# Optimization experiments

Hardware: AMD Instinct MI355X
Metric: run time of the kernel (lower is better)

The kernel has to match this reference:

```python
import jax, jax.numpy as jnp
import numpy as np

N, H, E, C, V, K = 4096, 256, 128, 32, 64, 20


def setup_inputs() -> dict:
    key = jax.random.key(0)
    ks = jax.random.split(key, 16)
    f = lambda k, s: jax.random.normal(k, s, dtype=jnp.float32)
    return {
        "vec": f(ks[0], (N, H)),
        "inp": f(ks[1], (N, E)),
        "h_prev": f(ks[2], (N, H)),
        "c_prev": f(ks[3], (N, H)),
        "Wlin": f(ks[4], (C, V, H)) * 0.05,
        "blin": f(ks[5], (C, V)) * 0.05,
        "Wec": f(ks[6], (2, H)) * 0.05,
        "bec": f(ks[7], (2,)) * 0.05,
        "Wrel": f(ks[8], (5, H)) * 0.05,
        "brel": f(ks[9], (5,)) * 0.05,
        "W_ih": f(ks[10], (K, 4 * H, E)) * 0.05,
        "b_ih": f(ks[11], (K, 4 * H)) * 0.05,
        "W_hh": f(ks[12], (K, 4 * H, H)) * 0.05,
        "b_hh": f(ks[13], (K, 4 * H)) * 0.05,
        "category": jax.random.randint(ks[14], (N,), 0, C, dtype=jnp.int32),
        "cell_id": jax.random.randint(ks[15], (N,), 0, K, dtype=jnp.int32),
        "true_idx": jax.random.randint(jax.random.fold_in(key, 100), (N,), 0, V, dtype=jnp.int32),
        "ec_idx": jax.random.randint(jax.random.fold_in(key, 101), (N,), 0, 2, dtype=jnp.int32),
        "rel_idx": jax.random.randint(jax.random.fold_in(key, 102), (N,), 0, 5, dtype=jnp.int32),
    }


def _ce(logits, targets):
    # per-row cross entropy (same math as nn.CrossEntropyLoss per example)
    logp = jax.nn.log_softmax(logits, axis=-1)
    return -jnp.take_along_axis(logp, targets[:, None], axis=-1)[:, 0]


def reference(vec, inp, h_prev, c_prev, Wlin, blin, Wec, bec, Wrel, brel,
              W_ih, b_ih, W_hh, b_hh, category, cell_id, true_idx, ec_idx, rel_idx):
    # --- get_log_odds: per-category tiny linear head, selected by category ---
    logits_all = jnp.einsum('nh,cvh->ncv', vec, Wlin) + blin          # [N,C,V]
    logits = jnp.take_along_axis(logits_all, category[:, None, None].astype(jnp.int32), axis=1)[:, 0]  # [N,V]
    logits_ec = vec @ Wec.T + bec                                      # [N,2]
    logits_rel = vec @ Wrel.T + brel                                   # [N,5]

    # --- calculate_loss: CE over valid children + ec + rel ---
    losses = _ce(logits, true_idx) + _ce(logits_ec, ec_idx) + _ce(logits_rel, rel_idx)  # [N]

    # --- get_next: per-child-index LSTMCell, selected by cell_id ---
    gates_all = (jnp.einsum('ne,kge->nkg', inp, W_ih)
                 + jnp.einsum('nh,kgh->nkg', h_prev, W_hh)
                 + b_ih + b_hh)                                        # [N,K,4H]
    gates = jnp.take_along_axis(gates_all, cell_id[:, None, None].astype(jnp.int32), axis=1)[:, 0]  # [N,4H]
    i, f, g, o = jnp.split(gates, 4, axis=-1)                          # torch LSTMCell gate order i,f,g,o
    c_next = jax.nn.sigmoid(f) * c_prev + jax.nn.sigmoid(i) * jnp.tanh(g)
    h_next = jax.nn.sigmoid(o) * jnp.tanh(c_next)

    # pack: [N, 1 + 2H] = loss | h_next | c_next
    return jnp.concatenate([losses[:, None], h_next, c_next], axis=-1)
```

## Files before the change

kernel.cpp:

```cpp
#include <hip/hip_runtime.h>
#include <hip/hip_bf16.h>
#include <math.h>

#define Nn 4096
#define Hdim 256
#define Edim 128
#define Cdim 32
#define Vdim 64
#define Kdim 20
#define G4H 1024
#define OUTS 513

#define SK 512
#define SC 256
#define RK_OFF 64
#define RC_OFF (RK_OFF + Kdim * SK)
#define NLI 18496
#define NSI 18497
#define ITL 18498
#define ITS (ITL + 640)

#define LSTM_REGION 592
#define LOSS_REGION 320
#define GRID (LSTM_REGION + LOSS_REGION)
#define XCHUNK 114

typedef short bf16x8 __attribute__((ext_vector_type(8)));
typedef float f32x4 __attribute__((ext_vector_type(4)));

__device__ __forceinline__ float sigmoidf_(float x) { return 1.0f / (1.0f + expf(-x)); }

__device__ __forceinline__ bf16x8 cvt8(float4 f0, float4 f1) {
    bf16x8 r;
    __hip_bfloat16 h;
    h = __float2bfloat16(f0.x); r[0] = *(short*)&h;
    h = __float2bfloat16(f0.y); r[1] = *(short*)&h;
    h = __float2bfloat16(f0.z); r[2] = *(short*)&h;
    h = __float2bfloat16(f0.w); r[3] = *(short*)&h;
    h = __float2bfloat16(f1.x); r[4] = *(short*)&h;
    h = __float2bfloat16(f1.y); r[5] = *(short*)&h;
    h = __float2bfloat16(f1.z); r[6] = *(short*)&h;
    h = __float2bfloat16(f1.w); r[7] = *(short*)&h;
    return r;
}

__device__ __forceinline__ void gl_lds16(const void* g, void* l) {
    __builtin_amdgcn_global_load_lds((const __attribute__((address_space(1))) void*)g,
                                     (__attribute__((address_space(3))) void*)l, 16, 0, 0);
}

__device__ __forceinline__ int swz(int r) { return ((r & 3) << 1) | ((r >> 2) & 1); }

__global__ __launch_bounds__(1024) void k_bucket(const int* __restrict__ cell_id,
                                                 const int* __restrict__ category,
                                                 int* __restrict__ ws) {
    __shared__ int cnt[32];
    __shared__ int off[33];
    int t = threadIdx.x;
    if (t < 32) cnt[t] = 0;
    __syncthreads();
    int i0 = t * 4;
    if (blockIdx.x == 0) {
        int4 v = ((const int4*)cell_id)[t];
        int r;
        r = atomicAdd(&cnt[v.x], 1); if (r < SK) ws[RK_OFF + v.x * SK + r] = i0 + 0;
        r = atomicAdd(&cnt[v.y], 1); if (r < SK) ws[RK_OFF + v.y * SK + r] = i0 + 1;
        r = atomicAdd(&cnt[v.z], 1); if (r < SK) ws[RK_OFF + v.z * SK + r] = i0 + 2;
        r = atomicAdd(&cnt[v.w], 1); if (r < SK) ws[RK_OFF + v.w * SK + r] = i0 + 3;
        __syncthreads();
        if (t == 0) {
            int a = 0;
            for (int kk = 0; kk < Kdim; kk++) { off[kk] = a; a += (min(cnt[kk], SK) + 31) >> 5; }
            ws[NLI] = a * 4;
        }
        __syncthreads();
        if (t < Kdim) {
            int ns = (min(cnt[t], SK) + 31) >> 5;
            int base = off[t] * 4;
            for (int hq = 0; hq < 4; hq++)
                for (int s = 0; s < ns; s++)
                    ws[ITL + base + hq * ns + s] = t | (s << 8) | (hq << 16);
        }
        if (t < 32) ws[t] = min(cnt[t], SK);
    } else {
        int4 v = ((const int4*)category)[t];
        int r;
        r = atomicAdd(&cnt[v.x], 1); if (r < SC) ws[RC_OFF + v.x * SC + r] = i0 + 0;
        r = atomicAdd(&cnt[v.y], 1); if (r < SC) ws[RC_OFF + v.y * SC + r] = i0 + 1;
        r = atomicAdd(&cnt[v.z], 1); if (r < SC) ws[RC_OFF + v.z * SC + r] = i0 + 2;
        r = atomicAdd(&cnt[v.w], 1); if (r < SC) ws[RC_OFF + v.w * SC + r] = i0 + 3;
        __syncthreads();
        if (t == 0) {
            int a = 0;
            for (int cc = 0; cc < Cdim; cc++) { off[cc] = a; a += (min(cnt[cc], SC) + 15) >> 4; }
            ws[NSI] = a;
        }
        __syncthreads();
        if (t < Cdim) {
            int ns = (min(cnt[t], SC) + 15) >> 4;
            int base = off[t];
            for (int s = 0; s < ns; s++)
                ws[ITS + base + s] = t | (s << 8);
        }
        if (t < 32) ws[32 + t] = min(cnt[t], SC);
    }
}

__global__ __launch_bounds__(256, 4) void k_main(
    const float* __restrict__ vec, const float* __restrict__ inp,
    const float* __restrict__ h_prev, const float* __restrict__ c_prev,
    const float* __restrict__ Wlin, const float* __restrict__ blin,
    const float* __restrict__ Wec, const float* __restrict__ bec,
    const float* __restrict__ Wrel, const float* __restrict__ brel,
    const float* __restrict__ W_ih, const float* __restrict__ b_ih,
    const float* __restrict__ W_hh, const float* __restrict__ b_hh,
    const int* __restrict__ true_idx, const int* __restrict__ ec_idx, const int* __restrict__ rel_idx,
    const int* __restrict__ ws,
    float* __restrict__ out)
{
    __shared__ __align__(16) char smem[36864];

    int t = threadIdx.x;
    int w = t >> 6, l = t & 63;
    int l15 = l & 15, quad = l >> 4;
    int lrow8 = l >> 3, lslot = l & 7;
    int p0 = (quad * 2) ^ swz(l15);

    int work = (blockIdx.x & 7) * XCHUNK + (blockIdx.x >> 3);

    if (work < LSTM_REGION) {
        if (work >= ws[NLI]) return;
        int item = ws[ITL + work];
        int k = item & 255, s = (item >> 8) & 255, hq = item >> 16;
        int cntk = ws[k];
        int rcount = min(32, cntk - s * 32);
        int reg_row = ws[RK_OFF + k * SK + s * 32 + min(l & 31, rcount - 1)];

        float* Wb = (float*)smem;
        float* Xb = (float*)(smem + 32768);
        const float* Wih_k = W_ih + (size_t)k * G4H * Edim;
        const float* Whh_k = W_hh + (size_t)k * G4H * Hdim;

        int xr = w * 8 + lrow8;
        int xrow = __shfl(reg_row, xr);
        int xg = lslot ^ swz(xr);

        int h = hq * 64 + w * 16 + l15;
        float bs[4];
        #pragma unroll
        for (int g = 0; g < 4; g++)
            bs[g] = b_ih[(size_t)k * G4H + g * Hdim + h] + b_hh[(size_t)k * G4H + g * Hdim + h];
        float cp[2][4];
        #pragma unroll
        for (int m = 0; m < 2; m++)
            #pragma unroll
            for (int reg = 0; reg < 4; reg++) {
                int r = m * 16 + quad * 4 + reg;
                int row = __shfl(reg_row, r);
                cp[m][reg] = c_prev[(size_t)row * Hdim + h];
            }

        f32x4 acc[2][4];
        #pragma unroll
        for (int m = 0; m < 2; m++)
            #pragma unroll
            for (int g = 0; g < 4; g++)
                acc[m][g] = (f32x4){0.f, 0.f, 0.f, 0.f};

        for (int st = 0; st < 12; st++) {
            int k0 = st * 32;
            const float* Wsrc; int stride, ko;
            if (k0 < Edim) { Wsrc = Wih_k; stride = Edim; ko = k0; }
            else           { Wsrc = Whh_k; stride = Hdim; ko = k0 - Edim; }
            __syncthreads();
            #pragma unroll
            for (int j = 0; j < 8; j++) {
                int r = w * 64 + j * 8 + lrow8;
                int g = lslot ^ swz(r);
                int gate = r >> 6, hl = r & 63;
                gl_lds16(Wsrc + (size_t)(gate * Hdim + hq * 64 + hl) * stride + ko + g * 4,
                         Wb + (w * 64 + j * 8) * 32);
            }
            {
                const float* Xs = (k0 < Edim) ? inp + (size_t)xrow * Edim + ko
                                              : h_prev + (size_t)xrow * Hdim + ko;
                gl_lds16(Xs + xg * 4, Xb + (w * 8) * 32);
            }
            __syncthreads();

            bf16x8 af[2], bfr[4];
            #pragma unroll
            for (int m = 0; m < 2; m++) {
                int row = m * 16 + l15;
                float4 lo = *(float4*)(Xb + row * 32 + p0 * 4);
                float4 hi = *(float4*)(Xb + row * 32 + (p0 ^ 1) * 4);
                af[m] = cvt8(lo, hi);
            }
            #pragma unroll
            for (int g = 0; g < 4; g++) {
                int row = g * 64 + w * 16 + l15;
                float4 lo = *(float4*)(Wb + row * 32 + p0 * 4);
                float4 hi = *(float4*)(Wb + row * 32 + (p0 ^ 1) * 4);
                bfr[g] = cvt8(lo, hi);
            }
            #pragma unroll
            for (int m = 0; m < 2; m++)
                #pragma unroll
                for (int g = 0; g < 4; g++)
                    acc[m][g] = __builtin_amdgcn_mfma_f32_16x16x32_bf16(af[m], bfr[g], acc[m][g], 0, 0, 0);
        }

        #pragma unroll
        for (int m = 0; m < 2; m++) {
            #pragma unroll
            for (int reg = 0; reg < 4; reg++) {
                int r = m * 16 + quad * 4 + reg;
                int row = __shfl(reg_row, r);
                if (r < rcount) {
                    float iv = acc[m][0][reg] + bs[0];
                    float fv = acc[m][1][reg] + bs[1];
                    float gv = acc[m][2][reg] + bs[2];
                    float ov = acc[m][3][reg] + bs[3];
                    float cn = sigmoidf_(fv) * cp[m][reg] + sigmoidf_(iv) * tanhf(gv);
                    float hn = sigmoidf_(ov) * tanhf(cn);
                    out[(size_t)row * OUTS + 1 + h] = hn;
                    out[(size_t)row * OUTS + 1 + Hdim + h] = cn;
                }
            }
        }
    } else {
        int work2 = work - LSTM_REGION;
        if (work2 >= ws[NSI]) return;
        int item = ws[ITS + work2];
        int c = item & 255, s = item >> 8;
        int cntc = ws[32 + c];
        int rcount = min(16, cntc - s * 16);
        int reg_row = ws[RC_OFF + c * SC + s * 16 + min(l & 15, rcount - 1)];

        float* Wb = (float*)smem;
        float* Vb = (float*)(smem + 10240);
        float* Lg = (float*)(smem + 12288);

        int xr = (w >= 2) ? ((w - 2) * 8 + lrow8) : 0;
        int xrow = __shfl(reg_row, xr);
        int xg = lslot ^ swz(xr);

        f32x4 a0 = (f32x4){0.f, 0.f, 0.f, 0.f};
        f32x4 a1 = (f32x4){0.f, 0.f, 0.f, 0.f};

        for (int st = 0; st < 8; st++) {
            int ko = st * 32;
            __syncthreads();
            for (int n = w; n < 10; n += 4) {
                int r = n * 8 + lrow8;
                int g = lslot ^ swz(r);
                const float* srcW;
                if (r < 64)      srcW = Wlin + ((size_t)c * Vdim + r) * Hdim;
                else if (r < 66) srcW = Wec + (size_t)(r - 64) * Hdim;
                else if (r < 71) srcW = Wrel + (size_t)(r - 66) * Hdim;
                else             srcW = Wlin + (size_t)c * Vdim * Hdim;
                gl_lds16(srcW + ko + g * 4, Wb + n * 8 * 32);
            }
            if (w >= 2)
                gl_lds16(vec + (size_t)xrow * Hdim + ko + xg * 4, Vb + ((w - 2) * 8) * 32);
            __syncthreads();

            bf16x8 af;
            {
                float4 lo = *(float4*)(Vb + l15 * 32 + p0 * 4);
                float4 hi = *(float4*)(Vb + l15 * 32 + (p0 ^ 1) * 4);
                af = cvt8(lo, hi);
            }
            {
                int row = w * 16 + l15;
                float4 lo = *(float4*)(Wb + row * 32 + p0 * 4);
                float4 hi = *(float4*)(Wb + row * 32 + (p0 ^ 1) * 4);
                bf16x8 b0 = cvt8(lo, hi);
                a0 = __builtin_amdgcn_mfma_f32_16x16x32_bf16(af, b0, a0, 0, 0, 0);
            }
            if (w == 3) {
                int row = 64 + l15;
                float4 lo = *(float4*)(Wb + row * 32 + p0 * 4);
                float4 hi = *(float4*)(Wb + row * 32 + (p0 ^ 1) * 4);
                bf16x8 b1 = cvt8(lo, hi);
                a1 = __builtin_amdgcn_mfma_f32_16x16x32_bf16(af, b1, a1, 0, 0, 0);
            }
        }
        __syncthreads();
        {
            int col = w * 16 + l15;
            float bb = blin[c * Vdim + col];
            #pragma unroll
            for (int reg = 0; reg < 4; reg++)
                Lg[(quad * 4 + reg) * 84 + col] = a0[reg] + bb;
            if (w == 3) {
                int col1 = 64 + l15;
                float bb1 = (l15 < 2) ? bec[l15] : ((l15 < 7) ? brel[l15 - 2] : 0.f);
                #pragma unroll
                for (int reg = 0; reg < 4; reg++)
                    Lg[(quad * 4 + reg) * 84 + col1] = a1[reg] + bb1;
            }
        }
        __syncthreads();
        for (int rr = 0; rr < 4; rr++) {
            int r = w * 4 + rr;
            if (r >= rcount) break;
            int orig = __shfl(reg_row, r);
            float lg = Lg[r * 84 + l];
            float mx = lg;
            for (int ss = 32; ss >= 1; ss >>= 1) mx = fmaxf(mx, __shfl_xor(mx, ss));
            float sm = expf(lg - mx);
            for (int ss = 32; ss >= 1; ss >>= 1) sm += __shfl_xor(sm, ss);
            float lt = __shfl(lg, true_idx[orig]);
            float loss = mx + logf(sm) - lt;
            if (l == 0) {
                float l0 = Lg[r * 84 + 64], l1 = Lg[r * 84 + 65];
                float me2 = fmaxf(l0, l1);
                loss += me2 + logf(expf(l0 - me2) + expf(l1 - me2)) - ((ec_idx[orig] == 0) ? l0 : l1);
                float rl[5] = { Lg[r * 84 + 66], Lg[r * 84 + 67], Lg[r * 84 + 68], Lg[r * 84 + 69], Lg[r * 84 + 70] };
                float mr = rl[0];
                #pragma unroll
                for (int i = 1; i < 5; i++) mr = fmaxf(mr, rl[i]);
                float sr = 0.f;
                #pragma unroll
                for (int i = 0; i < 5; i++) sr += expf(rl[i] - mr);
                loss += mr + logf(sr) - rl[rel_idx[orig]];
                out[(size_t)orig * OUTS] = loss;
            }
        }
    }
}

extern "C" void kernel_launch(void* const* d_in, const int* in_sizes, int n_in,
                              void* d_out, int out_size, void* d_ws, size_t ws_size,
                              hipStream_t stream) {
    const float* vec      = (const float*)d_in[0];
    const float* inp      = (const float*)d_in[1];
    const float* h_prev   = (const float*)d_in[2];
    const float* c_prev   = (const float*)d_in[3];
    const float* Wlin     = (const float*)d_in[4];
    const float* blin     = (const float*)d_in[5];
    const float* Wec      = (const float*)d_in[6];
    const float* bec      = (const float*)d_in[7];
    const float* Wrel     = (const float*)d_in[8];
    const float* brel     = (const float*)d_in[9];
    const float* W_ih     = (const float*)d_in[10];
    const float* b_ih     = (const float*)d_in[11];
    const float* W_hh     = (const float*)d_in[12];
    const float* b_hh     = (const float*)d_in[13];
    const int*   category = (const int*)d_in[14];
    const int*   cell_id  = (const int*)d_in[15];
    const int*   true_idx = (const int*)d_in[16];
    const int*   ec_idx   = (const int*)d_in[17];
    const int*   rel_idx  = (const int*)d_in[18];
    float* out = (float*)d_out;
    int* ws = (int*)d_ws;

    k_bucket<<<2, 1024, 0, stream>>>(cell_id, category, ws);
    k_main<<<GRID, 256, 0, stream>>>(
        vec, inp, h_prev, c_prev, Wlin, blin, Wec, bec, Wrel, brel,
        W_ih, b_ih, W_hh, b_hh, true_idx, ec_idx, rel_idx, ws, out);
}
```

Before: 150.1 us.

## Load LSTM activations directly into registers and reorder work items by slice

The activation tile no longer goes through LDS. Each lane loads its 8 fp32 values straight from global memory into registers and converts them to bf16 for the MFMA, which removes the X staging buffer and shrinks shared memory. Work items are now ordered so the four hq blocks that share the same rows are adjacent. Block-to-work mapping becomes identity instead of the XCD-interleaved chunking, and the c_prev load moves to the epilogue. The risks are that the uncoalesced per-lane global loads sit on the critical path before the barrier, and that dropping the XCD-aware mapping may reduce L2 locality.

```diff
diff --git a/kernel.cpp b/kernel.cpp
--- a/kernel.cpp
+++ b/kernel.cpp
@@ -23,7 +23,6 @@
 #define LSTM_REGION 592
 #define LOSS_REGION 320
 #define GRID (LSTM_REGION + LOSS_REGION)
-#define XCHUNK 114
 
 typedef short bf16x8 __attribute__((ext_vector_type(8)));
 typedef float f32x4 __attribute__((ext_vector_type(4)));
@@ -76,10 +75,10 @@
         __syncthreads();
         if (t < Kdim) {
             int ns = (min(cnt[t], SK) + 31) >> 5;
-            int base = off[t] * 4;
-            for (int hq = 0; hq < 4; hq++)
-                for (int s = 0; s < ns; s++)
-                    ws[ITL + base + hq * ns + s] = t | (s << 8) | (hq << 16);
+            int base = off[t];
+            for (int s = 0; s < ns; s++)
+                for (int hq = 0; hq < 4; hq++)
+                    ws[ITL + (base + s) * 4 + hq] = t | (s << 8) | (hq << 16);
         }
         if (t < 32) ws[t] = min(cnt[t], SK);
     } else {
@@ -118,7 +117,7 @@
     const int* __restrict__ ws,
     float* __restrict__ out)
 {
-    __shared__ __align__(16) char smem[36864];
+    __shared__ __align__(16) char smem[32768];
 
     int t = threadIdx.x;
     int w = t >> 6, l = t & 63;
@@ -126,7 +125,7 @@
     int lrow8 = l >> 3, lslot = l & 7;
     int p0 = (quad * 2) ^ swz(l15);
 
-    int work = (blockIdx.x & 7) * XCHUNK + (blockIdx.x >> 3);
+    int work = blockIdx.x;
 
     if (work < LSTM_REGION) {
         if (work >= ws[NLI]) return;
@@ -137,28 +136,21 @@
         int reg_row = ws[RK_OFF + k * SK + s * 32 + min(l & 31, rcount - 1)];
 
         float* Wb = (float*)smem;
-        float* Xb = (float*)(smem + 32768);
         const float* Wih_k = W_ih + (size_t)k * G4H * Edim;
         const float* Whh_k = W_hh + (size_t)k * G4H * Hdim;
 
-        int xr = w * 8 + lrow8;
-        int xrow = __shfl(reg_row, xr);
-        int xg = lslot ^ swz(xr);
+        int xrow0 = __shfl(reg_row, l15);
+        int xrow1 = __shfl(reg_row, 16 + l15);
+        const float* xi0 = inp + (size_t)xrow0 * Edim + quad * 8;
+        const float* xi1 = inp + (size_t)xrow1 * Edim + quad * 8;
+        const float* xh0 = h_prev + (size_t)xrow0 * Hdim + quad * 8;
+        const float* xh1 = h_prev + (size_t)xrow1 * Hdim + quad * 8;
 
         int h = hq * 64 + w * 16 + l15;
         float bs[4];
         #pragma unroll
         for (int g = 0; g < 4; g++)
             bs[g] = b_ih[(size_t)k * G4H + g * Hdim + h] + b_hh[(size_t)k * G4H + g * Hdim + h];
-        float cp[2][4];
-        #pragma unroll
-        for (int m = 0; m < 2; m++)
-            #pragma unroll
-            for (int reg = 0; reg < 4; reg++) {
-                int r = m * 16 + quad * 4 + reg;
-                int row = __shfl(reg_row, r);
-                cp[m][reg] = c_prev[(size_t)row * Hdim + h];
-            }
 
         f32x4 acc[2][4];
         #pragma unroll
@@ -181,21 +173,17 @@
                 gl_lds16(Wsrc + (size_t)(gate * Hdim + hq * 64 + hl) * stride + ko + g * 4,
                          Wb + (w * 64 + j * 8) * 32);
             }
-            {
-                const float* Xs = (k0 < Edim) ? inp + (size_t)xrow * Edim + ko
-                                              : h_prev + (size_t)xrow * Hdim + ko;
-                gl_lds16(Xs + xg * 4, Xb + (w * 8) * 32);
-            }
+            const float* px0 = (k0 < Edim) ? xi0 + k0 : xh0 + (k0 - Edim);
+            const float* px1 = (k0 < Edim) ? xi1 + k0 : xh1 + (k0 - Edim);
+            float4 fx00 = *(const float4*)(px0);
+            float4 fx01 = *(const float4*)(px0 + 4);
+            float4 fx10 = *(const float4*)(px1);
+            float4 fx11 = *(const float4*)(px1 + 4);
             __syncthreads();
 
             bf16x8 af[2], bfr[4];
-            #pragma unroll
-            for (int m = 0; m < 2; m++) {
-                int row = m * 16 + l15;
-                float4 lo = *(float4*)(Xb + row * 32 + p0 * 4);
-                float4 hi = *(float4*)(Xb + row * 32 + (p0 ^ 1) * 4);
-                af[m] = cvt8(lo, hi);
-            }
+            af[0] = cvt8(fx00, fx01);
+            af[1] = cvt8(fx10, fx11);
             #pragma unroll
             for (int g = 0; g < 4; g++) {
                 int row = g * 64 + w * 16 + l15;
@@ -221,7 +209,8 @@
                     float fv = acc[m][1][reg] + bs[1];
                     float gv = acc[m][2][reg] + bs[2];
                     float ov = acc[m][3][reg] + bs[3];
-                    float cn = sigmoidf_(fv) * cp[m][reg] + sigmoidf_(iv) * tanhf(gv);
+                    float cp = c_prev[(size_t)row * Hdim + h];
+                    float cn = sigmoidf_(fv) * cp + sigmoidf_(iv) * tanhf(gv);
                     float hn = sigmoidf_(ov) * tanhf(cn);
                     out[(size_t)row * OUTS + 1 + h] = hn;
                     out[(size_t)row * OUTS + 1 + Hdim + h] = cn;
```

Result: slower. 157.9 us (+5.2%).

## Overlap next-stage global-to-LDS loads with MFMA compute; reorder LSTM work items

Applied to the files above, without the earlier changes.

Both the LSTM and loss-head loops now read the current K-slice from LDS into registers, sync, and then issue the async global-to-LDS loads for the next slice before converting and running the MFMAs. A sched_barrier keeps the compiler from reordering the load issue past the compute. The goal is to hide global load latency behind compute without adding LDS buffers. Separately, the block-to-work mapping becomes identity and LSTM work items are ordered slice-major with the four h-quarters adjacent, so neighbouring blocks share input rows. This replaces the old XCD-strided chunking, which may change L2 locality across XCDs.

```diff
diff --git a/kernel.cpp b/kernel.cpp
--- a/kernel.cpp
+++ b/kernel.cpp
@@ -23,7 +23,6 @@
 #define LSTM_REGION 592
 #define LOSS_REGION 320
 #define GRID (LSTM_REGION + LOSS_REGION)
-#define XCHUNK 114
 
 typedef short bf16x8 __attribute__((ext_vector_type(8)));
 typedef float f32x4 __attribute__((ext_vector_type(4)));
@@ -76,10 +75,10 @@
         __syncthreads();
         if (t < Kdim) {
             int ns = (min(cnt[t], SK) + 31) >> 5;
-            int base = off[t] * 4;
-            for (int hq = 0; hq < 4; hq++)
-                for (int s = 0; s < ns; s++)
-                    ws[ITL + base + hq * ns + s] = t | (s << 8) | (hq << 16);
+            int base = off[t];
+            for (int s = 0; s < ns; s++)
+                for (int hq = 0; hq < 4; hq++)
+                    ws[ITL + (base + s) * 4 + hq] = t | (s << 8) | (hq << 16);
         }
         if (t < 32) ws[t] = min(cnt[t], SK);
     } else {
@@ -126,7 +125,7 @@
     int lrow8 = l >> 3, lslot = l & 7;
     int p0 = (quad * 2) ^ swz(l15);
 
-    int work = (blockIdx.x & 7) * XCHUNK + (blockIdx.x >> 3);
+    int work = blockIdx.x;
 
     if (work < LSTM_REGION) {
         if (work >= ws[NLI]) return;
@@ -167,47 +166,62 @@
             for (int g = 0; g < 4; g++)
                 acc[m][g] = (f32x4){0.f, 0.f, 0.f, 0.f};
 
+        #pragma unroll
+        for (int j = 0; j < 8; j++) {
+            int r = w * 64 + j * 8 + lrow8;
+            int g = lslot ^ swz(r);
+            int gate = r >> 6, hl = r & 63;
+            gl_lds16(Wih_k + (size_t)(gate * Hdim + hq * 64 + hl) * Edim + g * 4,
+                     Wb + (w * 64 + j * 8) * 32);
+        }
+        gl_lds16(inp + (size_t)xrow * Edim + xg * 4, Xb + (w * 8) * 32);
+        __syncthreads();
+
         for (int st = 0; st < 12; st++) {
-            int k0 = st * 32;
-            const float* Wsrc; int stride, ko;
-            if (k0 < Edim) { Wsrc = Wih_k; stride = Edim; ko = k0; }
-            else           { Wsrc = Whh_k; stride = Hdim; ko = k0 - Edim; }
-            __syncthreads();
-            #pragma unroll
-            for (int j = 0; j < 8; j++) {
-                int r = w * 64 + j * 8 + lrow8;
-                int g = lslot ^ swz(r);
-                int gate = r >> 6, hl = r & 63;
-                gl_lds16(Wsrc + (size_t)(gate * Hdim + hq * 64 + hl) * stride + ko + g * 4,
-                         Wb + (w * 64 + j * 8) * 32);
-            }
-            {
-                const float* Xs = (k0 < Edim) ? inp + (size_t)xrow * Edim + ko
-                                              : h_prev + (size_t)xrow * Hdim + ko;
-                gl_lds16(Xs + xg * 4, Xb + (w * 8) * 32);
-            }
-            __syncthreads();
-
-            bf16x8 af[2], bfr[4];
-            #pragma unroll
-            for (int m = 0; m < 2; m++) {
-                int row = m * 16 + l15;
-                float4 lo = *(float4*)(Xb + row * 32 + p0 * 4);
-                float4 hi = *(float4*)(Xb + row * 32 + (p0 ^ 1) * 4);
-                af[m] = cvt8(lo, hi);
-            }
+            float4 xlo0 = *(float4*)(Xb + l15 * 32 + p0 * 4);
+            float4 xhi0 = *(float4*)(Xb + l15 * 32 + (p0 ^ 1) * 4);
+            float4 xlo1 = *(float4*)(Xb + (16 + l15) * 32 + p0 * 4);
+            float4 xhi1 = *(float4*)(Xb + (16 + l15) * 32 + (p0 ^ 1) * 4);
+            float4 wlo[4], whi[4];
             #pragma unroll
             for (int g = 0; g < 4; g++) {
                 int row = g * 64 + w * 16 + l15;
-                float4 lo = *(float4*)(Wb + row * 32 + p0 * 4);
-                float4 hi = *(float4*)(Wb + row * 32 + (p0 ^ 1) * 4);
-                bfr[g] = cvt8(lo, hi);
-            }
+                wlo[g] = *(float4*)(Wb + row * 32 + p0 * 4);
+                whi[g] = *(float4*)(Wb + row * 32 + (p0 ^ 1) * 4);
+            }
+            __syncthreads();
+
+            if (st < 11) {
+                int k1 = (st + 1) * 32;
+                const float* Wsrc; int stride, ko;
+                if (k1 < Edim) { Wsrc = Wih_k; stride = Edim; ko = k1; }
+                else           { Wsrc = Whh_k; stride = Hdim; ko = k1 - Edim; }
+                #pragma unroll
+                for (int j = 0; j < 8; j++) {
+                    int r = w * 64 + j * 8 + lrow8;
+                    int g = lslot ^ swz(r);
+                    int gate = r >> 6, hl = r & 63;
+                    gl_lds16(Wsrc + (size_t)(gate * Hdim + hq * 64 + hl) * stride + ko + g * 4,
+                             Wb + (w * 64 + j * 8) * 32);
+                }
+                const float* Xs = (k1 < Edim) ? inp + (size_t)xrow * Edim + k1
+                                              : h_prev + (size_t)xrow * Hdim + (k1 - Edim);
+                gl_lds16(Xs + xg * 4, Xb + (w * 8) * 32);
+            }
+            __builtin_amdgcn_sched_barrier(0);
+
+            bf16x8 af[2], bfr[4];
+            af[0] = cvt8(xlo0, xhi0);
+            af[1] = cvt8(xlo1, xhi1);
+            #pragma unroll
+            for (int g = 0; g < 4; g++) bfr[g] = cvt8(wlo[g], whi[g]);
             #pragma unroll
             for (int m = 0; m < 2; m++)
                 #pragma unroll
                 for (int g = 0; g < 4; g++)
                     acc[m][g] = __builtin_amdgcn_mfma_f32_16x16x32_bf16(af[m], bfr[g], acc[m][g], 0, 0, 0);
+
+            if (st < 11) __syncthreads();
         }
 
         #pragma unroll
@@ -248,43 +262,63 @@
         f32x4 a0 = (f32x4){0.f, 0.f, 0.f, 0.f};
         f32x4 a1 = (f32x4){0.f, 0.f, 0.f, 0.f};
 
+        for (int n = w; n < 10; n += 4) {
+            int r = n * 8 + lrow8;
+            int g = lslot ^ swz(r);
+            const float* srcW;
+            if (r < 64)      srcW = Wlin + ((size_t)c * Vdim + r) * Hdim;
+            else if (r < 66) srcW = Wec + (size_t)(r - 64) * Hdim;
+            else if (r < 71) srcW = Wrel + (size_t)(r - 66) * Hdim;
+            else             srcW = Wlin + (size_t)c * Vdim * Hdim;
+            gl_lds16(srcW + g * 4, Wb + n * 8 * 32);
+        }
+        if (w >= 2)
+            gl_lds16(vec + (size_t)xrow * Hdim + xg * 4, Vb + ((w - 2) * 8) * 32);
+        __syncthreads();
+
         for (int st = 0; st < 8; st++) {
-            int ko = st * 32;
-            __syncthreads();
-            for (int n = w; n < 10; n += 4) {
-                int r = n * 8 + lrow8;
-                int g = lslot ^ swz(r);
-                const float* srcW;
-                if (r < 64)      srcW = Wlin + ((size_t)c * Vdim + r) * Hdim;
-                else if (r < 66) srcW = Wec + (size_t)(r - 64) * Hdim;
-                else if (r < 71) srcW = Wrel + (size_t)(r - 66) * Hdim;
-                else             srcW = Wlin + (size_t)c * Vdim * Hdim;
-                gl_lds16(srcW + ko + g * 4, Wb + n * 8 * 32);
-            }
-            if (w >= 2)
-                gl_lds16(vec + (size_t)xrow * Hdim + ko + xg * 4, Vb + ((w - 2) * 8) * 32);
-            __syncthreads();
-
-            bf16x8 af;
-            {
-                float4 lo = *(float4*)(Vb + l15 * 32 + p0 * 4);
-                float4 hi = *(float4*)(Vb + l15 * 32 + (p0 ^ 1) * 4);
-                af = cvt8(lo, hi);
-            }
+            float4 vlo = *(float4*)(Vb + l15 * 32 + p0 * 4);
+            float4 vhi = *(float4*)(Vb + l15 * 32 + (p0 ^ 1) * 4);
+            float4 w0lo, w0hi, w1lo, w1hi;
             {
                 int row = w * 16 + l15;
-                float4 lo = *(float4*)(Wb + row * 32 + p0 * 4);
-                float4 hi = *(float4*)(Wb + row * 32 + (p0 ^ 1) * 4);
-                bf16x8 b0 = cvt8(lo, hi);
-                a0 = __builtin_amdgcn_mfma_f32_16x16x32_bf16(af, b0, a0, 0, 0, 0);
+                w0lo = *(float4*)(Wb + row * 32 + p0 * 4);
+                w0hi = *(float4*)(Wb + row * 32 + (p0 ^ 1) * 4);
             }
             if (w == 3) {
                 int row = 64 + l15;
-                float4 lo = *(float4*)(Wb + row * 32 + p0 * 4);
-                float4 hi = *(float4*)(Wb + row * 32 + (p0 ^ 1) * 4);
-                bf16x8 b1 = cvt8(lo, hi);
+                w1lo = *(float4*)(Wb + row * 32 + p0 * 4);
+                w1hi = *(float4*)(Wb + row * 32 + (p0 ^ 1) * 4);
+            }
+            __syncthreads();
+
+            if (st < 7) {
+                int ko = (st + 1) * 32;
+                for (int n = w; n < 10; n += 4) {
+                    int r = n * 8 + lrow8;
+                    int g = lslot ^ swz(r);
+                    const float* srcW;
+                    if (r < 64)      srcW = Wlin + ((size_t)c * Vdim + r) * Hdim;
+                    else if (r < 66) srcW = Wec + (size_t)(r - 64) * Hdim;
+                    else if (r < 71) srcW = Wrel + (size_t)(r - 66) * Hdim;
+                    else             srcW = Wlin + (size_t)c * Vdim * Hdim;
+                    gl_lds16(srcW + ko + g * 4, Wb + n * 8 * 32);
+                }
+                if (w >= 2)
+                    gl_lds16(vec + (size_t)xrow * Hdim + ko + xg * 4, Vb + ((w - 2) * 8) * 32);
+            }
+            __builtin_amdgcn_sched_barrier(0);
+
+            bf16x8 af = cvt8(vlo, vhi);
+            {
+                bf16x8 b0 = cvt8(w0lo, w0hi);
+                a0 = __builtin_amdgcn_mfma_f32_16x16x32_bf16(af, b0, a0, 0, 0, 0);
+            }
+            if (w == 3) {
+                bf16x8 b1 = cvt8(w1lo, w1hi);
                 a1 = __builtin_amdgcn_mfma_f32_16x16x32_bf16(af, b1, a1, 0, 0, 0);
             }
+            if (st < 7) __syncthreads();
         }
         __syncthreads();
         {
```

New measurement: 147.5 us. About the same (-1.7%).
